# Optimization experiments

Measured on AMD Instinct MI355X. Metric: run time of the kernel, lower is better.

The kernel has to match this reference:

```python
import jax, jax.numpy as jnp
import numpy as np

N_NODES = 50000
N_EDGES = 800000
IN_FEATS = 32
OUT_FEATS = 32
NUM_HEADS = 4


def setup_inputs() -> dict:
    key = jax.random.key(0)
    ks = jax.random.split(key, 12)
    H, F, IN = NUM_HEADS, OUT_FEATS, IN_FEATS
    h = jax.random.normal(ks[0], (N_NODES, IN), dtype=jnp.float32)
    src = jax.random.randint(ks[1], (N_EDGES,), 0, N_NODES, dtype=jnp.int64)
    dst = jax.random.randint(ks[2], (N_EDGES,), 0, N_NODES, dtype=jnp.int64)
    s = 0.1
    W_gat = jax.random.normal(ks[3], (IN, H * F), dtype=jnp.float32) * s
    attn_l = jax.random.normal(ks[4], (H, F), dtype=jnp.float32) * s
    attn_r = jax.random.normal(ks[5], (H, F), dtype=jnp.float32) * s
    W_ih = jax.random.normal(ks[6], (3 * F, H * F), dtype=jnp.float32) * s
    W_hh = jax.random.normal(ks[7], (3 * F, F), dtype=jnp.float32) * s
    b_ih = jax.random.normal(ks[8], (3 * F,), dtype=jnp.float32) * s
    b_hh = jax.random.normal(ks[9], (3 * F,), dtype=jnp.float32) * s
    return {"h": h, "W_gat": W_gat, "attn_l": attn_l, "attn_r": attn_r,
            "W_ih": W_ih, "W_hh": W_hh, "b_ih": b_ih, "b_hh": b_hh,
            "src": src, "dst": dst}


def reference(h, W_gat, attn_l, attn_r, W_ih, W_hh, b_ih, b_hh, src, dst):
    N = h.shape[0]
    H, F = attn_l.shape
    # --- GATConv ---
    feat = (h @ W_gat).reshape(N, H, F)                      # (N,H,F)
    el = jnp.einsum('nhf,hf->nh', feat, attn_l)              # (N,H)
    er = jnp.einsum('nhf,hf->nh', feat, attn_r)              # (N,H)
    e = jax.nn.leaky_relu(el[src] + er[dst], 0.2)            # (E,H) edge logits
    emax = jax.ops.segment_max(e, dst, num_segments=N)       # per-dst max (stable)
    ee = jnp.exp(e - emax[dst])
    denom = jax.ops.segment_sum(ee, dst, num_segments=N)
    alpha = ee / denom[dst]                                  # segment softmax (E,H)
    msg = feat[src] * alpha[:, :, None]                      # (E,H,F)
    agg = jax.ops.segment_sum(msg, dst, num_segments=N)      # (N,H,F)
    x = agg.reshape(N, H * F)
    # --- GRUCell (torch semantics, gate order r,z,n) ---
    gi = x @ W_ih.T + b_ih                                   # (N,3F)
    gh = h @ W_hh.T + b_hh                                   # (N,3F)
    i_r, i_z, i_n = jnp.split(gi, 3, axis=1)
    h_r, h_z, h_n = jnp.split(gh, 3, axis=1)
    r = jax.nn.sigmoid(i_r + h_r)
    z = jax.nn.sigmoid(i_z + h_z)
    n = jnp.tanh(i_n + r * h_n)
    h_new = (1.0 - z) * n + z * h
    return jax.nn.elu(h_new)
```

## Files before the change

kernel.cpp:

```cpp
#include <hip/hip_runtime.h>
#include <hip/hip_bf16.h>
#include <cmath>

#define N_NODES 50000
#define N_EDGES 800000
#define CAP 64

#define NBINS 196
#define BIN_CAP 8192
#define CUR_PAD 32

#define WCB_ITEMS (144 * 32)
#define WCB_BLOCKS (WCB_ITEMS / 256)
#define WC_ITEMS (192 * 160)
#define WC_BLOCKS (WC_ITEMS / 256)

#define P1_EPT 8
#define P1_EPB (256 * P1_EPT)
#define P1_BLOCKS ((N_EDGES + P1_EPB - 1) / P1_EPB)
#define FEAT_BLOCKS ((N_NODES / 16 + 3) / 4)

typedef __attribute__((ext_vector_type(8))) short bf16x8;
typedef __attribute__((ext_vector_type(4))) float f32x4;

__device__ inline short bfbits(float x) {
    __hip_bfloat16 t = __float2bfloat16(x);
    return *reinterpret_cast<short*>(&t);
}

__device__ inline unsigned char f32_to_fp8(float x) {
    return (unsigned char)(__builtin_amdgcn_cvt_pk_fp8_f32(x, x, 0, false) & 0xff);
}

__global__ __launch_bounds__(256) void k_prep0(
        const float* __restrict__ Wg, const float* __restrict__ al,
        const float* __restrict__ ar, const float* __restrict__ Wih,
        const float* __restrict__ Whh, __hip_bfloat16* __restrict__ Wcomb,
        __hip_bfloat16* __restrict__ Wc, int* __restrict__ bin_cursor) {
    const int t = threadIdx.x;
    if (blockIdx.x < WCB_BLOCKS) {
        const int idx = blockIdx.x * 256 + t;
        const int row = idx >> 5, k = idx & 31;
        float v = 0.f;
        if (row < 128) {
            v = Wg[k * 128 + row];
        } else if (row < 136) {
            const int hd = (row - 128) & 3;
            const float* a = (row < 132) ? (al + hd * 32) : (ar + hd * 32);
            const float* w = Wg + k * 128 + hd * 32;
#pragma unroll
            for (int f = 0; f < 32; ++f) v = fmaf(w[f], a[f], v);
        }
        Wcomb[idx] = __float2bfloat16(v);
        return;
    }
    if (blockIdx.x < WCB_BLOCKS + WC_BLOCKS) {
        const int idx = (blockIdx.x - WCB_BLOCKS) * 256 + t;
        const int r = idx / 160, k = idx - r * 160;
        float v = 0.f;
        if (r < 96) { if (k < 128) v = Wih[r * 128 + k]; }
        else        { if (k >= 128) v = Whh[(r - 96) * 32 + (k - 128)]; }
        Wc[idx] = __float2bfloat16(v);
        return;
    }
    if (t < NBINS) bin_cursor[t * CUR_PAD] = 0;
}

__global__ __launch_bounds__(256) void k_part_feat(
        const float* __restrict__ h, const __hip_bfloat16* __restrict__ Wcomb,
        const int* __restrict__ src, const int* __restrict__ dst,
        int* __restrict__ bin_cursor, unsigned* __restrict__ bin_buf,
        unsigned char* __restrict__ feat, float* __restrict__ el,
        float* __restrict__ er) {
    const int t = threadIdx.x;
    if (blockIdx.x < P1_BLOCKS) {
        __shared__ int bcnt[256], bofs[256], cur[256], gbase[256];
        __shared__ int wt4[4];
        __shared__ unsigned stage[P1_EPB];
        bcnt[t] = 0;
        __syncthreads();
        int bn[P1_EPT];
        unsigned pk[P1_EPT];
        const int ebase = blockIdx.x * P1_EPB + t * P1_EPT;
        if (ebase < N_EDGES) {
            int dd[P1_EPT], ss[P1_EPT];
            *(int4*)(dd)     = *(const int4*)(dst + ebase);
            *(int4*)(dd + 4) = *(const int4*)(dst + ebase + 4);
            *(int4*)(ss)     = *(const int4*)(src + ebase);
            *(int4*)(ss + 4) = *(const int4*)(src + ebase + 4);
#pragma unroll
            for (int q = 0; q < P1_EPT; ++q) {
                bn[q] = dd[q] >> 8;
                pk[q] = (unsigned)ss[q] | ((unsigned)(dd[q] & 255) << 16);
                atomicAdd(&bcnt[bn[q]], 1);
            }
        } else {
#pragma unroll
            for (int q = 0; q < P1_EPT; ++q) bn[q] = -1;
        }
        __syncthreads();
        {
            const int wave = t >> 6, lane = t & 63;
            const int vv = bcnt[t];
            int x = vv;
#pragma unroll
            for (int m = 1; m < 64; m <<= 1) {
                const int y = __shfl_up(x, m, 64);
                if (lane >= m) x += y;
            }
            if (lane == 63) wt4[wave] = x;
            __syncthreads();
            int wb = 0;
#pragma unroll
            for (int i = 0; i < 4; ++i) if (i < wave) wb += wt4[i];
            const int off = wb + x - vv;
            bofs[t] = off;
            cur[t] = off;
            gbase[t] = (vv > 0) ? atomicAdd(&bin_cursor[t * CUR_PAD], vv) : 0;
        }
        __syncthreads();
#pragma unroll
        for (int q = 0; q < P1_EPT; ++q)
            if (bn[q] >= 0) stage[atomicAdd(&cur[bn[q]], 1)] = pk[q];
        __syncthreads();
        if (t < NBINS) {
            const int c = bcnt[t], o = bofs[t], g = gbase[t];
            unsigned* bb = bin_buf + (size_t)t * BIN_CAP;
            for (int j = 0; j < c; ++j) {
                const int gi = g + j;
                if (gi < BIN_CAP) bb[gi] = stage[o + j];
            }
        }
        return;
    }
    __shared__ unsigned char sbuf8[4][16][136];
    const int lane = t & 63, wave = t >> 6;
    const int li = lane & 15, quad = lane >> 4;
    const int mt = (blockIdx.x - P1_BLOCKS) * 4 + wave;
    if (mt >= N_NODES / 16) return;
    const int m_base = mt * 16;
    bf16x8 a;
    {
        const float4* hp = (const float4*)(h + (size_t)(m_base + li) * 32 + quad * 8);
        const float4 f0 = hp[0], f1 = hp[1];
        a[0] = bfbits(f0.x); a[1] = bfbits(f0.y); a[2] = bfbits(f0.z); a[3] = bfbits(f0.w);
        a[4] = bfbits(f1.x); a[5] = bfbits(f1.y); a[6] = bfbits(f1.z); a[7] = bfbits(f1.w);
    }
    f32x4 acc[9];
#pragma unroll
    for (int j = 0; j < 9; ++j) acc[j] = (f32x4){0.f, 0.f, 0.f, 0.f};
#pragma unroll
    for (int j = 0; j < 9; ++j) {
        const bf16x8 b = *(const bf16x8*)(Wcomb + (size_t)(j * 16 + li) * 32 + quad * 8);
        acc[j] = __builtin_amdgcn_mfma_f32_16x16x32_bf16(a, b, acc[j], 0, 0, 0);
    }
#pragma unroll
    for (int j = 0; j < 8; ++j)
#pragma unroll
        for (int i = 0; i < 4; ++i)
            sbuf8[wave][quad * 4 + i][j * 16 + li] = f32_to_fp8(acc[j][i]);
    __builtin_amdgcn_wave_barrier();
#pragma unroll
    for (int rep = 0; rep < 4; ++rep) {
        const int row = rep * 4 + quad;
        const unsigned long long v = *(const unsigned long long*)(&sbuf8[wave][row][li * 8]);
        *(unsigned long long*)(feat + (size_t)(m_base + row) * 128 + li * 8) = v;
    }
    if (li < 8) {
#pragma unroll
        for (int i = 0; i < 4; ++i) {
            const int m = m_base + quad * 4 + i;
            if (li < 4) el[m * 4 + li] = acc[8][i];
            else        er[m * 4 + (li - 4)] = acc[8][i];
        }
    }
}

__global__ __launch_bounds__(256) void k_scat2(
        const int* __restrict__ bin_cursor, const unsigned* __restrict__ bin_buf,
        int* __restrict__ srcs_p, int* __restrict__ counts) {
    __shared__ int lcnt[256];
    const int t = threadIdx.x;
    const int b = blockIdx.x;
    lcnt[t] = 0;
    __syncthreads();
    const int cb = min(bin_cursor[b * CUR_PAD], BIN_CAP);
    const uint4* bb4 = (const uint4*)(bin_buf + (size_t)b * BIN_CAP);
    for (int i = t * 4; i < cb; i += 1024) {
        const uint4 p4 = bb4[i >> 2];
#pragma unroll
        for (int k = 0; k < 4; ++k) {
            if (i + k < cb) {
                const unsigned p = (&p4.x)[k];
                const int dl = p >> 16;
                const int s = p & 0xffff;
                const int pos = atomicAdd(&lcnt[dl], 1);
                if (pos < CAP) srcs_p[(size_t)(b * 256 + dl) * CAP + pos] = s;
            }
        }
    }
    __syncthreads();
    const int node = b * 256 + t;
    if (node < N_NODES) counts[node] = lcnt[t];
}

__global__ __launch_bounds__(1024, 8) void k_aggr_gru(
        const int* __restrict__ counts, const int* __restrict__ srcs_p,
        const unsigned char* __restrict__ feat,
        const float* __restrict__ el, const float* __restrict__ er,
        const float* __restrict__ h, const __hip_bfloat16* __restrict__ Wc,
        const float* __restrict__ bih, const float* __restrict__ bhh,
        float* __restrict__ out) {
    __shared__ __hip_bfloat16 xh_tile[16][160];
    __shared__ int   sl_s[16][64];
    __shared__ float eel_s[16][64];
    __shared__ float ex[2][3][16][16];
    const int wave = threadIdx.x >> 6;
    const int lane = threadIdx.x & 63;
    const int eh = lane >> 5;
    const int fl = lane & 31;
    const int hq = fl >> 3;
    const int mbase = blockIdx.x * 16;
    const int n = mbase + wave;
    int* sl = sl_s[wave];
    float* eel = eel_s[wave];

    const int cnt = min(counts[n], CAP);
    sl[lane] = srcs_p[(size_t)n * CAP + lane];
    const float ern = er[n * 4 + (lane & 3)];
    __builtin_amdgcn_wave_barrier();

    float a0 = 0.f, a1 = 0.f, a2 = 0.f, a3 = 0.f, psum = 0.f;
    for (int i = 0; i < cnt; i += 16) {
        int sj[8];
#pragma unroll
        for (int j = 0; j < 8; ++j) {
            const int e2 = i + 2 * j + eh;
            sj[j] = sl[e2 < cnt ? e2 : 0];
        }
        unsigned uq[8];
#pragma unroll
        for (int j = 0; j < 8; ++j)
            uq[j] = *(const unsigned*)(feat + (size_t)sj[j] * 128 + fl * 4);
        const int eedge = i + (lane >> 2);
        const int sle = sl[eedge < cnt ? eedge : 0];
        float v = el[sle * 4 + (lane & 3)] + ern;
        v = v > 0.f ? v : 0.2f * v;
        const float wl = (eedge < cnt) ? __expf(v) : 0.f;
        psum += wl;
        eel[lane] = wl;
        __builtin_amdgcn_wave_barrier();
#pragma unroll
        for (int j = 0; j < 8; ++j) {
            const float w = eel[((2 * j + eh) << 2) | hq];
            a0 = fmaf(w, __builtin_amdgcn_cvt_f32_fp8(uq[j], 0), a0);
            a1 = fmaf(w, __builtin_amdgcn_cvt_f32_fp8(uq[j], 1), a1);
            a2 = fmaf(w, __builtin_amdgcn_cvt_f32_fp8(uq[j], 2), a2);
            a3 = fmaf(w, __builtin_amdgcn_cvt_f32_fp8(uq[j], 3), a3);
        }
        __builtin_amdgcn_wave_barrier();
    }
    a0 += __shfl_xor(a0, 32, 64);
    a1 += __shfl_xor(a1, 32, 64);
    a2 += __shfl_xor(a2, 32, 64);
    a3 += __shfl_xor(a3, 32, 64);
#pragma unroll
    for (int m = 4; m < 64; m <<= 1) psum += __shfl_xor(psum, m, 64);
    const float dn = __shfl(psum, hq, 64);
    const float inv = (cnt > 0) ? 1.f / dn : 0.f;
    if (lane < 32) {
        __hip_bfloat162 p0, p1;
        p0.x = __float2bfloat16(a0 * inv); p0.y = __float2bfloat16(a1 * inv);
        p1.x = __float2bfloat16(a2 * inv); p1.y = __float2bfloat16(a3 * inv);
        __hip_bfloat162* xp = (__hip_bfloat162*)&xh_tile[wave][0];
        xp[lane * 2]     = p0;
        xp[lane * 2 + 1] = p1;
        xh_tile[wave][128 + lane] = __float2bfloat16(h[(size_t)n * 32 + lane]);
    }
    __syncthreads();

    if (wave < 4) {
        const int li = lane & 15, quad = lane >> 4;
        const int cb = wave >> 1;
        const int ghrole = wave & 1;
        bf16x8 a[5];
#pragma unroll
        for (int s = 0; s < 5; ++s)
            a[s] = *(const bf16x8*)((const char*)&xh_tile[0][0] + li * 320 + s * 64 + quad * 16);
        f32x4 acc[3];
#pragma unroll
        for (int g = 0; g < 3; ++g) {
            acc[g] = (f32x4){0.f, 0.f, 0.f, 0.f};
            const int j = g * 2 + cb + ghrole * 6;
            const bf16x8* bp = (const bf16x8*)(Wc + (size_t)(j * 16 + li) * 160 + quad * 8);
            acc[g] = __builtin_amdgcn_mfma_f32_16x16x32_bf16(a[0], bp[0],  acc[g], 0, 0, 0);
            acc[g] = __builtin_amdgcn_mfma_f32_16x16x32_bf16(a[1], bp[4],  acc[g], 0, 0, 0);
            acc[g] = __builtin_amdgcn_mfma_f32_16x16x32_bf16(a[2], bp[8],  acc[g], 0, 0, 0);
            acc[g] = __builtin_amdgcn_mfma_f32_16x16x32_bf16(a[3], bp[12], acc[g], 0, 0, 0);
            acc[g] = __builtin_amdgcn_mfma_f32_16x16x32_bf16(a[4], bp[16], acc[g], 0, 0, 0);
        }
        if (ghrole) {
#pragma unroll
            for (int g = 0; g < 3; ++g)
#pragma unroll
                for (int i = 0; i < 4; ++i)
                    ex[cb][g][quad * 4 + i][li] = acc[g][i];
        }
        __syncthreads();
        if (!ghrole) {
            const int c = cb * 16 + li;
            const float bir = bih[c],      bhr = bhh[c];
            const float biz = bih[32 + c], bhz = bhh[32 + c];
            const float bin = bih[64 + c], bhn = bhh[64 + c];
#pragma unroll
            for (int i = 0; i < 4; ++i) {
                const int row = quad * 4 + i;
                const int m = mbase + row;
                const float gr = acc[0][i] + bir + ex[cb][0][row][li] + bhr;
                const float gz = acc[1][i] + biz + ex[cb][1][row][li] + bhz;
                const float r = 1.f / (1.f + expf(-gr));
                const float z = 1.f / (1.f + expf(-gz));
                const float nn = tanhf(acc[2][i] + bin + r * (ex[cb][2][row][li] + bhn));
                const float hv = h[(size_t)m * 32 + c];
                const float hn = (1.f - z) * nn + z * hv;
                out[(size_t)m * 32 + c] = hn > 0.f ? hn : expm1f(hn);
            }
        }
    } else {
        __syncthreads();
    }
}

extern "C" void kernel_launch(void* const* d_in, const int* in_sizes, int n_in,
                              void* d_out, int out_size, void* d_ws, size_t ws_size,
                              hipStream_t stream) {
    const float* h   = (const float*)d_in[0];
    const float* Wg  = (const float*)d_in[1];
    const float* al  = (const float*)d_in[2];
    const float* ar  = (const float*)d_in[3];
    const float* Wih = (const float*)d_in[4];
    const float* Whh = (const float*)d_in[5];
    const float* bih = (const float*)d_in[6];
    const float* bhh = (const float*)d_in[7];
    const int* src   = (const int*)d_in[8];
    const int* dst   = (const int*)d_in[9];
    float* out = (float*)d_out;

    float* el = (float*)d_ws;
    float* er = el + (size_t)N_NODES * 4;
    unsigned char* feat8 = (unsigned char*)(er + (size_t)N_NODES * 4);
    __hip_bfloat16* Wc    = (__hip_bfloat16*)(feat8 + (size_t)N_NODES * 128);
    __hip_bfloat16* Wcomb = Wc + 192 * 160;
    int* counts  = (int*)(Wcomb + WCB_ITEMS);
    int* srcs_p  = counts + N_NODES;
    int* bin_cursor = srcs_p + (size_t)N_NODES * CAP;
    unsigned* bin_buf = (unsigned*)(bin_cursor + NBINS * CUR_PAD);

    k_prep0<<<WCB_BLOCKS + WC_BLOCKS + 1, 256, 0, stream>>>(
        Wg, al, ar, Wih, Whh, Wcomb, Wc, bin_cursor);
    k_part_feat<<<P1_BLOCKS + FEAT_BLOCKS, 256, 0, stream>>>(
        h, Wcomb, src, dst, bin_cursor, bin_buf, feat8, el, er);
    k_scat2<<<NBINS, 256, 0, stream>>>(bin_cursor, bin_buf, srcs_p, counts);
    k_aggr_gru<<<N_NODES / 16, 1024, 0, stream>>>(
        counts, srcs_p, feat8, el, er, h, Wc, bih, bhh, out);
}
```

Baseline: 153.7 us.

## Fuse bin scatter into aggregation kernel using shared-memory adjacency lists

Removes the separate scatter kernel. Each aggregation block now reads its destination bin directly and builds per-node source lists in LDS before the attention aggregation and GRU. This avoids writing and rereading the padded global adjacency array and saves one launch. In exchange, each bin is scanned by four blocks, each wave handles four nodes in turn, and the larger LDS footprint lowers occupancy.

```diff
diff --git a/kernel.cpp b/kernel.cpp
--- a/kernel.cpp
+++ b/kernel.cpp
@@ -19,6 +19,7 @@
 #define P1_EPB (256 * P1_EPT)
 #define P1_BLOCKS ((N_EDGES + P1_EPB - 1) / P1_EPB)
 #define FEAT_BLOCKS ((N_NODES / 16 + 3) / 4)
+#define AGGR_BLOCKS 782
 
 typedef __attribute__((ext_vector_type(8))) short bf16x8;
 typedef __attribute__((ext_vector_type(4))) float f32x4;
@@ -176,122 +177,122 @@
     }
 }
 
-__global__ __launch_bounds__(256) void k_scat2(
+__global__ __launch_bounds__(1024) void k_aggr_gru(
         const int* __restrict__ bin_cursor, const unsigned* __restrict__ bin_buf,
-        int* __restrict__ srcs_p, int* __restrict__ counts) {
-    __shared__ int lcnt[256];
-    const int t = threadIdx.x;
-    const int b = blockIdx.x;
-    lcnt[t] = 0;
-    __syncthreads();
-    const int cb = min(bin_cursor[b * CUR_PAD], BIN_CAP);
-    const uint4* bb4 = (const uint4*)(bin_buf + (size_t)b * BIN_CAP);
-    for (int i = t * 4; i < cb; i += 1024) {
-        const uint4 p4 = bb4[i >> 2];
-#pragma unroll
-        for (int k = 0; k < 4; ++k) {
-            if (i + k < cb) {
-                const unsigned p = (&p4.x)[k];
-                const int dl = p >> 16;
-                const int s = p & 0xffff;
-                const int pos = atomicAdd(&lcnt[dl], 1);
-                if (pos < CAP) srcs_p[(size_t)(b * 256 + dl) * CAP + pos] = s;
-            }
-        }
-    }
-    __syncthreads();
-    const int node = b * 256 + t;
-    if (node < N_NODES) counts[node] = lcnt[t];
-}
-
-__global__ __launch_bounds__(1024, 8) void k_aggr_gru(
-        const int* __restrict__ counts, const int* __restrict__ srcs_p,
         const unsigned char* __restrict__ feat,
         const float* __restrict__ el, const float* __restrict__ er,
         const float* __restrict__ h, const __hip_bfloat16* __restrict__ Wc,
         const float* __restrict__ bih, const float* __restrict__ bhh,
         float* __restrict__ out) {
-    __shared__ __hip_bfloat16 xh_tile[16][160];
-    __shared__ int   sl_s[16][64];
+    __shared__ unsigned short list[64][CAP];
+    __shared__ int lcnt[64];
+    __shared__ __hip_bfloat16 xh_tile[64][160];
     __shared__ float eel_s[16][64];
-    __shared__ float ex[2][3][16][16];
-    const int wave = threadIdx.x >> 6;
-    const int lane = threadIdx.x & 63;
+    __shared__ float ex[4][2][3][16][16];
+    const int t = threadIdx.x;
+    const int wave = t >> 6, lane = t & 63;
+    const int pb = blockIdx.x >> 2, sub = blockIdx.x & 3;
+    const int nodebase = blockIdx.x * 64;
+
+    if (t < 64) lcnt[t] = 0;
+    __syncthreads();
+
+    const int cb = min(bin_cursor[pb * CUR_PAD], BIN_CAP);
+    const uint4* bb4 = (const uint4*)(bin_buf + (size_t)pb * BIN_CAP);
+    for (int i = t * 4; i < cb; i += 4096) {
+        const uint4 p4 = bb4[i >> 2];
+#pragma unroll
+        for (int k = 0; k < 4; ++k) {
+            if (i + k < cb) {
+                const unsigned p = (&p4.x)[k];
+                const int local = (p >> 16) & 255;
+                if ((local >> 6) == sub) {
+                    const int dl = local & 63;
+                    const int pos = atomicAdd(&lcnt[dl], 1);
+                    if (pos < CAP) list[dl][pos] = (unsigned short)(p & 0xffff);
+                }
+            }
+        }
+    }
+    __syncthreads();
+
     const int eh = lane >> 5;
     const int fl = lane & 31;
     const int hq = fl >> 3;
-    const int mbase = blockIdx.x * 16;
-    const int n = mbase + wave;
-    int* sl = sl_s[wave];
     float* eel = eel_s[wave];
-
-    const int cnt = min(counts[n], CAP);
-    sl[lane] = srcs_p[(size_t)n * CAP + lane];
-    const float ern = er[n * 4 + (lane & 3)];
-    __builtin_amdgcn_wave_barrier();
-
-    float a0 = 0.f, a1 = 0.f, a2 = 0.f, a3 = 0.f, psum = 0.f;
-    for (int i = 0; i < cnt; i += 16) {
-        int sj[8];
-#pragma unroll
-        for (int j = 0; j < 8; ++j) {
-            const int e2 = i + 2 * j + eh;
-            sj[j] = sl[e2 < cnt ? e2 : 0];
-        }
-        unsigned uq[8];
-#pragma unroll
-        for (int j = 0; j < 8; ++j)
-            uq[j] = *(const unsigned*)(feat + (size_t)sj[j] * 128 + fl * 4);
-        const int eedge = i + (lane >> 2);
-        const int sle = sl[eedge < cnt ? eedge : 0];
-        float v = el[sle * 4 + (lane & 3)] + ern;
-        v = v > 0.f ? v : 0.2f * v;
-        const float wl = (eedge < cnt) ? __expf(v) : 0.f;
-        psum += wl;
-        eel[lane] = wl;
-        __builtin_amdgcn_wave_barrier();
-#pragma unroll
-        for (int j = 0; j < 8; ++j) {
-            const float w = eel[((2 * j + eh) << 2) | hq];
-            a0 = fmaf(w, __builtin_amdgcn_cvt_f32_fp8(uq[j], 0), a0);
-            a1 = fmaf(w, __builtin_amdgcn_cvt_f32_fp8(uq[j], 1), a1);
-            a2 = fmaf(w, __builtin_amdgcn_cvt_f32_fp8(uq[j], 2), a2);
-            a3 = fmaf(w, __builtin_amdgcn_cvt_f32_fp8(uq[j], 3), a3);
-        }
-        __builtin_amdgcn_wave_barrier();
-    }
-    a0 += __shfl_xor(a0, 32, 64);
-    a1 += __shfl_xor(a1, 32, 64);
-    a2 += __shfl_xor(a2, 32, 64);
-    a3 += __shfl_xor(a3, 32, 64);
-#pragma unroll
-    for (int m = 4; m < 64; m <<= 1) psum += __shfl_xor(psum, m, 64);
-    const float dn = __shfl(psum, hq, 64);
-    const float inv = (cnt > 0) ? 1.f / dn : 0.f;
-    if (lane < 32) {
-        __hip_bfloat162 p0, p1;
-        p0.x = __float2bfloat16(a0 * inv); p0.y = __float2bfloat16(a1 * inv);
-        p1.x = __float2bfloat16(a2 * inv); p1.y = __float2bfloat16(a3 * inv);
-        __hip_bfloat162* xp = (__hip_bfloat162*)&xh_tile[wave][0];
-        xp[lane * 2]     = p0;
-        xp[lane * 2 + 1] = p1;
-        xh_tile[wave][128 + lane] = __float2bfloat16(h[(size_t)n * 32 + lane]);
+    for (int u = 0; u < 4; ++u) {
+        const int row = wave * 4 + u;
+        const int n = nodebase + row;
+        const int nvalid = (n < N_NODES);
+        const int nc = nvalid ? n : (N_NODES - 1);
+        const int cnt = min(lcnt[row], CAP);
+        const unsigned short* sl = list[row];
+        const float ern = er[(size_t)nc * 4 + (lane & 3)];
+        float a0 = 0.f, a1 = 0.f, a2 = 0.f, a3 = 0.f, psum = 0.f;
+        for (int i = 0; i < cnt; i += 16) {
+            int sj[8];
+#pragma unroll
+            for (int j = 0; j < 8; ++j) {
+                const int e2 = i + 2 * j + eh;
+                sj[j] = sl[e2 < cnt ? e2 : 0];
+            }
+            unsigned uq[8];
+#pragma unroll
+            for (int j = 0; j < 8; ++j)
+                uq[j] = *(const unsigned*)(feat + (size_t)sj[j] * 128 + fl * 4);
+            const int eedge = i + (lane >> 2);
+            const int sle = sl[eedge < cnt ? eedge : 0];
+            float v = el[(size_t)sle * 4 + (lane & 3)] + ern;
+            v = v > 0.f ? v : 0.2f * v;
+            const float wl = (eedge < cnt) ? __expf(v) : 0.f;
+            psum += wl;
+            eel[lane] = wl;
+            __builtin_amdgcn_wave_barrier();
+#pragma unroll
+            for (int j = 0; j < 8; ++j) {
+                const float w = eel[((2 * j + eh) << 2) | hq];
+                a0 = fmaf(w, __builtin_amdgcn_cvt_f32_fp8(uq[j], 0), a0);
+                a1 = fmaf(w, __builtin_amdgcn_cvt_f32_fp8(uq[j], 1), a1);
+                a2 = fmaf(w, __builtin_amdgcn_cvt_f32_fp8(uq[j], 2), a2);
+                a3 = fmaf(w, __builtin_amdgcn_cvt_f32_fp8(uq[j], 3), a3);
+            }
+            __builtin_amdgcn_wave_barrier();
+        }
+        a0 += __shfl_xor(a0, 32, 64);
+        a1 += __shfl_xor(a1, 32, 64);
+        a2 += __shfl_xor(a2, 32, 64);
+        a3 += __shfl_xor(a3, 32, 64);
+#pragma unroll
+        for (int m = 4; m < 64; m <<= 1) psum += __shfl_xor(psum, m, 64);
+        const float dn = __shfl(psum, hq, 64);
+        const float inv = (cnt > 0) ? 1.f / dn : 0.f;
+        if (lane < 32) {
+            __hip_bfloat162 p0, p1;
+            p0.x = __float2bfloat16(a0 * inv); p0.y = __float2bfloat16(a1 * inv);
+            p1.x = __float2bfloat16(a2 * inv); p1.y = __float2bfloat16(a3 * inv);
+            __hip_bfloat162* xp = (__hip_bfloat162*)&xh_tile[row][0];
+            xp[lane * 2]     = p0;
+            xp[lane * 2 + 1] = p1;
+            xh_tile[row][128 + lane] = nvalid ?
+                __float2bfloat16(h[(size_t)n * 32 + lane]) : __float2bfloat16(0.f);
+        }
     }
     __syncthreads();
 
-    if (wave < 4) {
+    {
         const int li = lane & 15, quad = lane >> 4;
-        const int cb = wave >> 1;
+        const int tt = wave >> 2;
+        const int cbk = (wave >> 1) & 1;
         const int ghrole = wave & 1;
         bf16x8 a[5];
 #pragma unroll
         for (int s = 0; s < 5; ++s)
-            a[s] = *(const bf16x8*)((const char*)&xh_tile[0][0] + li * 320 + s * 64 + quad * 16);
+            a[s] = *(const bf16x8*)((const char*)&xh_tile[tt * 16][0] + li * 320 + s * 64 + quad * 16);
         f32x4 acc[3];
 #pragma unroll
         for (int g = 0; g < 3; ++g) {
             acc[g] = (f32x4){0.f, 0.f, 0.f, 0.f};
-            const int j = g * 2 + cb + ghrole * 6;
+            const int j = g * 2 + cbk + ghrole * 6;
             const bf16x8* bp = (const bf16x8*)(Wc + (size_t)(j * 16 + li) * 160 + quad * 8);
             acc[g] = __builtin_amdgcn_mfma_f32_16x16x32_bf16(a[0], bp[0],  acc[g], 0, 0, 0);
             acc[g] = __builtin_amdgcn_mfma_f32_16x16x32_bf16(a[1], bp[4],  acc[g], 0, 0, 0);
@@ -304,30 +305,30 @@
             for (int g = 0; g < 3; ++g)
 #pragma unroll
                 for (int i = 0; i < 4; ++i)
-                    ex[cb][g][quad * 4 + i][li] = acc[g][i];
+                    ex[tt][cbk][g][quad * 4 + i][li] = acc[g][i];
         }
         __syncthreads();
         if (!ghrole) {
-            const int c = cb * 16 + li;
+            const int c = cbk * 16 + li;
             const float bir = bih[c],      bhr = bhh[c];
             const float biz = bih[32 + c], bhz = bhh[32 + c];
             const float bin = bih[64 + c], bhn = bhh[64 + c];
 #pragma unroll
             for (int i = 0; i < 4; ++i) {
                 const int row = quad * 4 + i;
-                const int m = mbase + row;
-                const float gr = acc[0][i] + bir + ex[cb][0][row][li] + bhr;
-                const float gz = acc[1][i] + biz + ex[cb][1][row][li] + bhz;
-                const float r = 1.f / (1.f + expf(-gr));
-                const float z = 1.f / (1.f + expf(-gz));
-                const float nn = tanhf(acc[2][i] + bin + r * (ex[cb][2][row][li] + bhn));
-                const float hv = h[(size_t)m * 32 + c];
-                const float hn = (1.f - z) * nn + z * hv;
-                out[(size_t)m * 32 + c] = hn > 0.f ? hn : expm1f(hn);
-            }
-        }
-    } else {
-        __syncthreads();
+                const int m = nodebase + tt * 16 + row;
+                if (m < N_NODES) {
+                    const float gr = acc[0][i] + bir + ex[tt][cbk][0][row][li] + bhr;
+                    const float gz = acc[1][i] + biz + ex[tt][cbk][1][row][li] + bhz;
+                    const float r = 1.f / (1.f + expf(-gr));
+                    const float z = 1.f / (1.f + expf(-gz));
+                    const float nn = tanhf(acc[2][i] + bin + r * (ex[tt][cbk][2][row][li] + bhn));
+                    const float hv = h[(size_t)m * 32 + c];
+                    const float hn = (1.f - z) * nn + z * hv;
+                    out[(size_t)m * 32 + c] = hn > 0.f ? hn : expm1f(hn);
+                }
+            }
+        }
     }
 }
 
@@ -351,16 +352,13 @@
     unsigned char* feat8 = (unsigned char*)(er + (size_t)N_NODES * 4);
     __hip_bfloat16* Wc    = (__hip_bfloat16*)(feat8 + (size_t)N_NODES * 128);
     __hip_bfloat16* Wcomb = Wc + 192 * 160;
-    int* counts  = (int*)(Wcomb + WCB_ITEMS);
-    int* srcs_p  = counts + N_NODES;
-    int* bin_cursor = srcs_p + (size_t)N_NODES * CAP;
+    int* bin_cursor = (int*)(Wcomb + WCB_ITEMS);
     unsigned* bin_buf = (unsigned*)(bin_cursor + NBINS * CUR_PAD);
 
     k_prep0<<<WCB_BLOCKS + WC_BLOCKS + 1, 256, 0, stream>>>(
         Wg, al, ar, Wih, Whh, Wcomb, Wc, bin_cursor);
     k_part_feat<<<P1_BLOCKS + FEAT_BLOCKS, 256, 0, stream>>>(
         h, Wcomb, src, dst, bin_cursor, bin_buf, feat8, el, er);
-    k_scat2<<<NBINS, 256, 0, stream>>>(bin_cursor, bin_buf, srcs_p, counts);
-    k_aggr_gru<<<N_NODES / 16, 1024, 0, stream>>>(
-        counts, srcs_p, feat8, el, er, h, Wc, bih, bhh, out);
-}
+    k_aggr_gru<<<AGGR_BLOCKS, 1024, 0, stream>>>(
+        bin_cursor, bin_buf, feat8, el, er, h, Wc, bih, bhh, out);
+}
```

Measured after the change: 162.5 us. 1.06x slower.
